# Optimization experiments

Measured on AMD Instinct MI355X. Metric: run time of the kernel, lower is better.

## Reference

```python
import jax, jax.numpy as jnp
import numpy as np

ALPHA = 0.5
INV_COEFF = 25.0
STD_COEFF = 25.0
COV_COEFF = 1.0
NUM_MATCHES = 50
EPS = 1e-5
GAMMA = 1.0


def _cdist(a, b):
    # (B,M,C),(B,N,C) -> (B,M,N) euclidean, matmul-based like torch.cdist
    a2 = jnp.sum(a * a, axis=-1, keepdims=True)            # (B,M,1)
    b2 = jnp.sum(b * b, axis=-1, keepdims=True)            # (B,N,1)
    d2 = a2 + jnp.swapaxes(b2, -1, -2) - 2.0 * jnp.einsum('bmc,bnc->bmn', a, b)
    return jnp.sqrt(jnp.maximum(d2, 0.0))


def _nn_match(input_maps, candidate_maps, distances, num_matches):
    # topk(k=1, largest=False) == min/argmin over last dim
    nn_dists = jnp.min(distances, axis=-1)                 # (B,M)
    nn_indices = jnp.argmin(distances, axis=-1)            # (B,M)
    # k smallest nn_dists, ascending order
    _, best_input_idx = jax.lax.top_k(-nn_dists, num_matches)   # (B,k)
    best_cand_idx = jnp.take_along_axis(nn_indices, best_input_idx, axis=1)
    filt_in = jnp.take_along_axis(input_maps, best_input_idx[:, :, None], axis=1)
    filt_cand = jnp.take_along_axis(candidate_maps, best_cand_idx[:, :, None], axis=1)
    return filt_in, filt_cand


def _off_diag_sq_sum(c):
    return jnp.sum(c * c) - jnp.sum(jnp.diag(c) ** 2)


def _std_term(x_flat):
    # unbiased variance over sample dim (torch var default)
    std = jnp.sqrt(jnp.var(x_flat, axis=0, ddof=1) + EPS)
    return jnp.mean(jax.nn.relu(GAMMA - std)) / 2.0


def _cov_term(x_flat):
    n, c = x_flat.shape
    xc = x_flat - jnp.mean(x_flat, axis=0)
    cov = xc.T @ xc / (n - 1)
    return _off_diag_sq_sum(cov) / c


def _vicreg_global(x, y):
    inv = jnp.mean((x - y) ** 2)
    std = _std_term(x) + _std_term(y)
    cov = _cov_term(x) + _cov_term(y)
    return INV_COEFF * inv + STD_COEFF * std + COV_COEFF * cov


def _vicregl_maps(x, y):
    # x, y: (B, k, C)
    inv = jnp.mean((x - y) ** 2)
    xf = x.reshape(-1, x.shape[-1])
    yf = y.reshape(-1, y.shape[-1])
    std = _std_term(xf) + _std_term(yf)
    cov = _cov_term(xf) + _cov_term(yf)
    return INV_COEFF * inv, STD_COEFF * std, COV_COEFF * cov


def _local_loss(spatial_1, spatial_2):
    B, C, H, W = spatial_1.shape
    maps_1 = spatial_1.reshape(B, C, H * W).transpose(0, 2, 1)   # (B,HW,C)
    maps_2 = spatial_2.reshape(B, C, H * W).transpose(0, 2, 1)
    d12 = _cdist(maps_1, maps_2)
    m1f, m1n = _nn_match(maps_1, maps_2, d12, NUM_MATCHES)
    d21 = _cdist(maps_2, maps_1)
    m2f, m2n = _nn_match(maps_2, maps_1, d21, NUM_MATCHES)
    inv1, var1, cov1 = _vicregl_maps(m1f, m1n)
    inv2, var2, cov2 = _vicregl_maps(m2f, m2n)
    return (inv1 + inv2) / 2 + (var1 + var2) / 2 + (cov1 + cov2) / 2


def setup_inputs() -> dict:
    key = jax.random.key(0)
    k1, k2, k3, k4 = jax.random.split(key, 4)
    B, C, H, W = 64, 768, 24, 24
    return {
        'spatial_1': jax.random.normal(k1, (B, C, H, W), dtype=jnp.float32),
        'pooled_1': jax.random.normal(k2, (B, C), dtype=jnp.float32),
        'spatial_2': jax.random.normal(k3, (B, C, H, W), dtype=jnp.float32),
        'pooled_2': jax.random.normal(k4, (B, C), dtype=jnp.float32),
    }


def reference(spatial_1, pooled_1, spatial_2, pooled_2):
    global_loss = _vicreg_global(pooled_1, pooled_2)
    local_loss = _local_loss(spatial_1, spatial_2)
    return ALPHA * global_loss + (1.0 - ALPHA) * local_loss
```

## Files before the change

kernel.cpp:

```cpp
#include <hip/hip_runtime.h>
#include <stdint.h>

typedef unsigned long long ull;
typedef unsigned int uint;
typedef unsigned short ushort;

typedef __attribute__((ext_vector_type(8))) short short8;
typedef __attribute__((ext_vector_type(4))) float floatx4;

#define B   64
#define C   768
#define HW  576
#define K   50
#define NLOC (B*K)

#define OFF_SLOTS   0
#define OFF_COLSUM  256
#define OFF_NN1     18688
#define OFF_NN2     313600
#define OFF_SELP    608512
#define OFF_SELQ    634112
#define OFF_XT      954624
#define OFF_MP      OFF_XT
#define OFF_XGT     114200832
#define OFF_M       133861632

#define SLOT_INVG 0
#define SLOT_STD  1
#define SLOT_COV  7
#define SLOT_INV1 13
#define SLOT_INV2 14

__device__ __forceinline__ ull umin64(ull a, ull b) { return a < b ? a : b; }

__device__ __forceinline__ float bf2f_lo(uint u) { return __uint_as_float(u << 16); }
__device__ __forceinline__ float bf2f_hi(uint u) { return __uint_as_float(u & 0xffff0000u); }
__device__ __forceinline__ float bf2f(ushort u) { return __uint_as_float(((uint)u) << 16); }

__device__ __forceinline__ ushort f2bf(float f) {
    uint u = __float_as_uint(f);
    uint r = (u + 0x7fffu + ((u >> 16) & 1u)) >> 16;
    return (ushort)r;
}

__device__ __forceinline__ float blk_reduce_sum(float v, float* s4) {
    for (int off = 32; off > 0; off >>= 1) v += __shfl_down(v, off, 64);
    int lane = threadIdx.x & 63, w = threadIdx.x >> 6;
    if (lane == 0) s4[w] = v;
    __syncthreads();
    float r = 0.f;
    if (threadIdx.x == 0) r = s4[0] + s4[1] + s4[2] + s4[3];
    return r;
}

__global__ __launch_bounds__(256) void convert_kernel(const float* __restrict__ x1,
                                                      const float* __restrict__ x2,
                                                      ushort* __restrict__ xT,
                                                      float* __restrict__ normp) {
    int z = blockIdx.y;
    int which = z >> 6, b = z & 63;
    int half = blockIdx.x & 1;
    int pt = blockIdx.x >> 1;
    int p0 = pt * 64, c0 = half * 384;
    const float* X = (which ? x2 : x1) + ((size_t)b * C + c0) * HW + p0;

    __shared__ ushort tile[64][392];
    __shared__ float nlds[64][4];

    int t = threadIdx.x;
    int pq = t & 15, cq = t >> 4;
    int w = t >> 6;

    float ss[4] = {0.f, 0.f, 0.f, 0.f};

#pragma unroll
    for (int pass = 0; pass < 6; ++pass) {
        floatx4 v[4];
#pragma unroll
        for (int i = 0; i < 4; ++i)
            v[i] = *(const floatx4*)(X + (size_t)(pass * 64 + 4 * cq + i) * HW + 4 * pq);
#pragma unroll
        for (int j = 0; j < 4; ++j) {
            ushort u0 = f2bf(v[0][j]), u1 = f2bf(v[1][j]);
            ushort u2 = f2bf(v[2][j]), u3 = f2bf(v[3][j]);
            ushort4 uu; uu.x = u0; uu.y = u1; uu.z = u2; uu.w = u3;
            *(ushort4*)&tile[4 * pq + j][pass * 64 + 4 * cq] = uu;
            float r0 = bf2f(u0), r1 = bf2f(u1), r2 = bf2f(u2), r3 = bf2f(u3);
            ss[j] = fmaf(r0, r0, ss[j]); ss[j] = fmaf(r1, r1, ss[j]);
            ss[j] = fmaf(r2, r2, ss[j]); ss[j] = fmaf(r3, r3, ss[j]);
        }
    }
#pragma unroll
    for (int j = 0; j < 4; ++j) {
        ss[j] += __shfl_xor(ss[j], 16, 64);
        ss[j] += __shfl_xor(ss[j], 32, 64);
    }
    if ((t & 63) < 16) {
#pragma unroll
        for (int j = 0; j < 4; ++j) nlds[4 * pq + j][w] = ss[j];
    }
    __syncthreads();

    ushort* dst = xT + (((size_t)which * B + b) * HW + p0) * C + c0;
    const char* tb = (const char*)tile;
#pragma unroll
    for (int step = 0; step < 12; ++step) {
        int ib = (step * 256 + t) * 16;
        int p = ib / 768, cb = ib % 768;
        short8 vv = *(const short8*)(tb + (size_t)p * 784 + cb);
        *(short8*)(dst + (size_t)p * C + (cb >> 1)) = vv;
    }
    if (t < 64) {
        float nv = nlds[t][0] + nlds[t][1] + nlds[t][2] + nlds[t][3];
        normp[((size_t)half * 128 + which * 64 + b) * HW + p0 + t] = nv;
    }
}

template<int NG>
__device__ __forceinline__ void gemm_pp(const ushort* const (&gA)[2], const ushort* const (&gB)[2],
                                        char* pool, int w,
                                        const int (&offA)[4], const int (&offB)[4],
                                        floatx4 (&acc)[4][4]) {
    auto issue = [&](int h) {
        char* buf = pool + (h & 3) * 16384;
#pragma unroll
        for (int n = 0; n < 2; ++n) {
            __builtin_amdgcn_global_load_lds(
                (const __attribute__((address_space(1))) void*)(gA[n] + h * 32),
                (__attribute__((address_space(3))) void*)(buf + w * 2048 + n * 1024), 16, 0, 0);
            __builtin_amdgcn_global_load_lds(
                (const __attribute__((address_space(1))) void*)(gB[n] + h * 32),
                (__attribute__((address_space(3))) void*)(buf + 8192 + w * 2048 + n * 1024), 16, 0, 0);
        }
    };
    issue(0); issue(1); issue(2);
    for (int h = 0; h < NG; ++h) {
        if (h < NG - 2)      asm volatile("s_waitcnt vmcnt(8)" ::: "memory");
        else if (h == NG - 2) asm volatile("s_waitcnt vmcnt(4)" ::: "memory");
        else                  asm volatile("s_waitcnt vmcnt(0)" ::: "memory");
        __builtin_amdgcn_s_barrier();
        if (h + 3 < NG) issue(h + 3);
        __builtin_amdgcn_sched_barrier(0);
        const char* buf = pool + (h & 3) * 16384;
        short8 a[4], bb[4];
#pragma unroll
        for (int i = 0; i < 4; ++i) a[i] = *(const short8*)(buf + offA[i]);
#pragma unroll
        for (int j = 0; j < 4; ++j) bb[j] = *(const short8*)(buf + 8192 + offB[j]);
#pragma unroll
        for (int i = 0; i < 4; ++i)
#pragma unroll
            for (int j = 0; j < 4; ++j)
                acc[i][j] = __builtin_amdgcn_mfma_f32_16x16x32_bf16(a[i], bb[j], acc[i][j], 0, 0, 0);
    }
}

__global__ __launch_bounds__(256) void cdist_mfma(const ushort* __restrict__ xT,
                                                  const float* __restrict__ normp,
                                                  ull* __restrict__ nn1,
                                                  ull* __restrict__ nn2) {
    int id = blockIdx.x;
    int xcd = id & 7, slot = id >> 3;
    int b = xcd + 8 * (slot / 25);
    int t = slot % 25;
    int qt = t % 5, pt = t / 5;

    const ushort* X1 = xT + (size_t)b * HW * C;
    const ushort* X2 = xT + (size_t)(B + b) * HW * C;

    __shared__ ull pool[8192];
    char* poolc = (char*)pool;

    int tid = threadIdx.x;
    int w = tid >> 6, l = tid & 63;
    int quad = l >> 4, col = l & 15;
    int lrow = l >> 2, pos = l & 3;

    const ushort* gA[2]; const ushort* gB[2];
#pragma unroll
    for (int n = 0; n < 2; ++n) {
        int sm = w * 32 + n * 16 + lrow;
        int cdat = pos ^ ((sm >> 1) & 3);
        int p = pt * 128 + sm; if (p >= HW) p = HW - 1;
        int q = qt * 128 + sm; if (q >= HW) q = HW - 1;
        gA[n] = X1 + (size_t)p * C + cdat * 8;
        gB[n] = X2 + (size_t)q * C + cdat * 8;
    }

    int offA[4], offB[4];
#pragma unroll
    for (int i = 0; i < 4; ++i) {
        int m_loc = (w >> 1) * 64 + i * 16 + col;
        offA[i] = m_loc * 64 + ((quad ^ ((m_loc >> 1) & 3)) * 16);
        int n_loc = (w & 1) * 64 + i * 16 + col;
        offB[i] = n_loc * 64 + ((quad ^ ((n_loc >> 1) & 3)) * 16);
    }

    floatx4 zero = {0.f, 0.f, 0.f, 0.f};
    floatx4 acc[4][4];
#pragma unroll
    for (int i = 0; i < 4; ++i)
#pragma unroll
        for (int j = 0; j < 4; ++j) acc[i][j] = zero;

    gemm_pp<24>(gA, gB, poolc, w, offA, offB, acc);

    const float* n1a = normp + (size_t)b * HW;
    const float* n1b = normp + (size_t)(128 + b) * HW;
    const float* n2a = normp + (size_t)(64 + b) * HW;
    const float* n2b = normp + (size_t)(192 + b) * HW;
    float n1v[4][4]; bool vp[4][4];
    float n2v[4];    bool vq[4];
#pragma unroll
    for (int i = 0; i < 4; ++i)
#pragma unroll
        for (int r = 0; r < 4; ++r) {
            int p = pt * 128 + (w >> 1) * 64 + i * 16 + quad * 4 + r;
            vp[i][r] = (p < HW);
            int pc = p < HW ? p : (HW - 1);
            n1v[i][r] = n1a[pc] + n1b[pc];
        }
#pragma unroll
    for (int j = 0; j < 4; ++j) {
        int q = qt * 128 + (w & 1) * 64 + j * 16 + col;
        vq[j] = (q < HW);
        int qc = q < HW ? q : (HW - 1);
        n2v[j] = n2a[qc] + n2b[qc];
    }

    __syncthreads();
    typedef ull row33[33];
    row33* red = (row33*)pool;

#pragma unroll
    for (int i = 0; i < 4; ++i)
#pragma unroll
        for (int r = 0; r < 4; ++r) {
            int p_loc = (w >> 1) * 64 + i * 16 + quad * 4 + r;
            ull best = ~0ull;
#pragma unroll
            for (int j = 0; j < 4; ++j) {
                if (!vq[j]) continue;
                float d2 = fmaxf(n1v[i][r] + n2v[j] - 2.0f * acc[i][j][r], 0.0f);
                unsigned q_glob = qt * 128 + (w & 1) * 64 + j * 16 + col;
                best = umin64(best, ((ull)__float_as_uint(d2) << 32) | q_glob);
            }
            red[p_loc][(w & 1) * 16 + col] = best;
        }
    __syncthreads();
    if (tid < 128) {
        int p_glob = pt * 128 + tid;
        ull m = ~0ull;
#pragma unroll
        for (int x = 0; x < 32; ++x) m = umin64(m, red[tid][x]);
        if (p_glob < HW) atomicMin(&nn1[(size_t)b * HW + p_glob], m);
    }
    __syncthreads();
#pragma unroll
    for (int j = 0; j < 4; ++j) {
        int q_loc = (w & 1) * 64 + j * 16 + col;
        ull best = ~0ull;
#pragma unroll
        for (int i = 0; i < 4; ++i)
#pragma unroll
            for (int r = 0; r < 4; ++r) {
                if (!vp[i][r]) continue;
                float d2 = fmaxf(n1v[i][r] + n2v[j] - 2.0f * acc[i][j][r], 0.0f);
                unsigned p_glob = pt * 128 + (w >> 1) * 64 + i * 16 + quad * 4 + r;
                best = umin64(best, ((ull)__float_as_uint(d2) << 32) | p_glob);
            }
        red[q_loc][(w >> 1) * 4 + quad] = best;
    }
    __syncthreads();
    if (tid < 128) {
        int q_glob = qt * 128 + tid;
        ull m = ~0ull;
#pragma unroll
        for (int x = 0; x < 8; ++x) m = umin64(m, red[tid][x]);
        if (q_glob < HW) atomicMin(&nn2[(size_t)b * HW + q_glob], m);
    }
}

__global__ __launch_bounds__(64) void select_topk_wave(const ull* __restrict__ nn1,
                                                       const ull* __restrict__ nn2,
                                                       int* __restrict__ sel_p,
                                                       int* __restrict__ sel_q) {
    int b = blockIdx.x, dir = blockIdx.y;
    const ull* nn = dir ? nn2 : nn1;
    int lane = threadIdx.x;
    ull key[9]; uint qv[9];
#pragma unroll
    for (int r = 0; r < 9; ++r) {
        int p = r * 64 + lane;
        ull e = nn[(size_t)b * HW + p];
        key[r] = (e & 0xFFFFFFFF00000000ull) | (unsigned)p;
        qv[r] = (uint)(e & 0xFFFFFFFFu);
    }
    int* sp = sel_p + (dir * B + b) * K;
    int* sq = sel_q + (dir * B + b) * K;
    for (int it = 0; it < K; ++it) {
        ull m = key[0];
#pragma unroll
        for (int r = 1; r < 9; ++r) m = umin64(m, key[r]);
#pragma unroll
        for (int off = 32; off > 0; off >>= 1) m = umin64(m, __shfl_xor(m, off, 64));
#pragma unroll
        for (int r = 0; r < 9; ++r) {
            if (key[r] == m) {
                sp[it] = (int)(uint)(m & 0xFFFFFFFFu);
                sq[it] = (int)qv[r];
                key[r] = ~0ull;
            }
        }
    }
}

__global__ __launch_bounds__(256) void gather_jmajor(const ushort* __restrict__ xT,
                                                     const int* __restrict__ sel_p,
                                                     const int* __restrict__ sel_q,
                                                     ushort* __restrict__ XgT) {
    int j = blockIdx.x, s = blockIdx.y;
    int dir = s >> 1;
    int whichsrc = (s == 1 || s == 2) ? 1 : 0;
    const int* sel = (s & 1) ? sel_q : sel_p;
    __shared__ int sidx[64];
    __shared__ uint buf[64][33];
    int tid = threadIdx.x;
    if (tid < 64) sidx[tid] = sel[(dir * B + tid) * K + j];
    __syncthreads();
    int rb = tid >> 2, u = tid & 3;
    const ushort* srow = xT + (((size_t)whichsrc * B + rb) * HW + sidx[rb]) * C;
    int wv = tid >> 6, lb = tid & 63;
    ushort* obase = XgT + (size_t)s * C * NLOC + (size_t)j * 64 + lb;
    for (int ch = 0; ch < 12; ++ch) {
        __syncthreads();
        uint4 v0 = *(const uint4*)(srow + ch * 64 + u * 8);
        uint4 v1 = *(const uint4*)(srow + ch * 64 + (u + 4) * 8);
        buf[rb][u * 4 + 0] = v0.x; buf[rb][u * 4 + 1] = v0.y;
        buf[rb][u * 4 + 2] = v0.z; buf[rb][u * 4 + 3] = v0.w;
        buf[rb][(u + 4) * 4 + 0] = v1.x; buf[rb][(u + 4) * 4 + 1] = v1.y;
        buf[rb][(u + 4) * 4 + 2] = v1.z; buf[rb][(u + 4) * 4 + 3] = v1.w;
        __syncthreads();
#pragma unroll
        for (int st = 0; st < 16; ++st) {
            int cl = wv + st * 4;
            uint uv = buf[lb][cl >> 1];
            ushort val = (cl & 1) ? (ushort)(uv >> 16) : (ushort)(uv & 0xffffu);
            obase[(size_t)(ch * 64 + cl) * NLOC] = val;
        }
    }
}

__global__ __launch_bounds__(256) void ata_mfma(const ushort* __restrict__ XgT,
                                                float* __restrict__ Mp) {
    int bx = blockIdx.x;
    int mat = blockIdx.y, split = blockIdx.z;
    int rt = bx / 6, ct = bx % 6;
    const ushort* X = XgT + (size_t)mat * C * NLOC;

    __shared__ ull pool[8192];
    char* poolc = (char*)pool;

    int tid = threadIdx.x;
    int w = tid >> 6, l = tid & 63;
    int quad = l >> 4, col = l & 15;
    int lrow = l >> 2, pos = l & 3;

    const ushort* gA[2]; const ushort* gB[2];
#pragma unroll
    for (int n = 0; n < 2; ++n) {
        int sm = w * 32 + n * 16 + lrow;
        int cdat = pos ^ ((sm >> 1) & 3);
        gA[n] = X + (size_t)(rt * 128 + sm) * NLOC + split * 640 + cdat * 8;
        gB[n] = X + (size_t)(ct * 128 + sm) * NLOC + split * 640 + cdat * 8;
    }

    int offA[4], offB[4];
#pragma unroll
    for (int i = 0; i < 4; ++i) {
        int m_loc = (w >> 1) * 64 + i * 16 + col;
        offA[i] = m_loc * 64 + ((quad ^ ((m_loc >> 1) & 3)) * 16);
        int n_loc = (w & 1) * 64 + i * 16 + col;
        offB[i] = n_loc * 64 + ((quad ^ ((n_loc >> 1) & 3)) * 16);
    }

    floatx4 zero = {0.f, 0.f, 0.f, 0.f};
    floatx4 acc[4][4];
#pragma unroll
    for (int i = 0; i < 4; ++i)
#pragma unroll
        for (int j = 0; j < 4; ++j) acc[i][j] = zero;

    gemm_pp<20>(gA, gB, poolc, w, offA, offB, acc);

    float* Mo = Mp + (size_t)(mat * 5 + split) * C * C;
#pragma unroll
    for (int i = 0; i < 4; ++i)
#pragma unroll
        for (int j = 0; j < 4; ++j)
#pragma unroll
            for (int r = 0; r < 4; ++r) {
                int row = rt * 128 + (w >> 1) * 64 + i * 16 + quad * 4 + r;
                int cc  = ct * 128 + (w & 1) * 64 + j * 16 + col;
                Mo[(size_t)row * C + cc] = acc[i][j][r];
            }
}

__global__ __launch_bounds__(256) void ata_pooled(const float* __restrict__ p1,
                                                  const float* __restrict__ p2,
                                                  float* __restrict__ M) {
    int mat = 4 + blockIdx.z;
    const float* X = (mat == 4) ? p1 : p2;
    int n = B;
    float* Mo = M + (size_t)mat * C * C;
    int ct = blockIdx.x, rt = blockIdx.y;

    __shared__ float As[16][64];
    __shared__ float Bs[16][64];
    int tid = threadIdx.x;
    int tx = tid & 15, ty = tid >> 4;
    int lr = tid >> 4, lc = (tid & 15) * 4;

    float acc[4][4] = {};
    for (int k0 = 0; k0 < n; k0 += 16) {
        float4 av = *(const float4*)&X[(size_t)(k0 + lr) * C + rt * 64 + lc];
        float4 bv = *(const float4*)&X[(size_t)(k0 + lr) * C + ct * 64 + lc];
        __syncthreads();
        *(float4*)&As[lr][lc] = av;
        *(float4*)&Bs[lr][lc] = bv;
        __syncthreads();
#pragma unroll
        for (int kk = 0; kk < 16; ++kk) {
            float4 af = *(const float4*)&As[kk][ty * 4];
            float4 bf = *(const float4*)&Bs[kk][tx * 4];
            float a[4] = {af.x, af.y, af.z, af.w};
            float bb[4] = {bf.x, bf.y, bf.z, bf.w};
#pragma unroll
            for (int i = 0; i < 4; ++i)
#pragma unroll
                for (int j = 0; j < 4; ++j)
                    acc[i][j] = fmaf(a[i], bb[j], acc[i][j]);
        }
    }
#pragma unroll
    for (int i = 0; i < 4; ++i) {
        float4 o = {acc[i][0], acc[i][1], acc[i][2], acc[i][3]};
        *(float4*)&Mo[(size_t)(rt * 64 + ty * 4 + i) * C + ct * 64 + tx * 4] = o;
    }
}

__global__ __launch_bounds__(256) void colsum4_kernel(const ushort* __restrict__ XgT,
                                                      float* __restrict__ colsum) {
    int mat = blockIdx.y, cb = blockIdx.x * 4;
    int r = threadIdx.x >> 6, lane = threadIdx.x & 63;
    const ushort* row = XgT + ((size_t)mat * C + cb + r) * NLOC;
    float s = 0.f;
    for (int i = lane; i < NLOC; i += 64) s += bf2f(row[i]);
    for (int off = 32; off > 0; off >>= 1) s += __shfl_down(s, off, 64);
    if (lane == 0) colsum[mat * C + cb + r] = s;
}

__global__ __launch_bounds__(256) void colsum_pooled(const float* __restrict__ p1,
                                                     const float* __restrict__ p2,
                                                     float* __restrict__ colsum) {
    int mat = 4 + blockIdx.y;
    const float* X = (mat == 4) ? p1 : p2;
    int c = blockIdx.x * 256 + threadIdx.x;
    float s = 0.f;
    for (int r = 0; r < B; ++r) s += X[(size_t)r * C + c];
    colsum[mat * C + c] = s;
}

__global__ __launch_bounds__(256) void std_kernel(const float* __restrict__ Mp,
                                                  const float* __restrict__ M,
                                                  const float* __restrict__ colsum,
                                                  float* __restrict__ slots) {
    int mat = blockIdx.y;
    float n = (mat < 4) ? (float)NLOC : (float)B;
    int c = blockIdx.x * 256 + threadIdx.x;
    float r = 0.f;
    if (c < C) {
        float mcc;
        if (mat < 4) {
            mcc = 0.f;
#pragma unroll
            for (int s = 0; s < 5; ++s)
                mcc += Mp[(size_t)(mat * 5 + s) * C * C + (size_t)c * C + c];
        } else {
            mcc = M[(size_t)mat * C * C + (size_t)c * C + c];
        }
        float cs = colsum[mat * C + c];
        float var = (mcc - cs * cs / n) / (n - 1.0f);
        float sd = sqrtf(var + 1e-5f);
        float g = 1.0f - sd;
        r = g > 0.f ? g : 0.f;
    }
    __shared__ float s4[4];
    float t = blk_reduce_sum(r, s4);
    if (threadIdx.x == 0) atomicAdd(&slots[SLOT_STD + mat], t);
}

__global__ __launch_bounds__(256) void cov_kernel(const float* __restrict__ Mp,
                                                  const float* __restrict__ M,
                                                  const float* __restrict__ colsum,
                                                  float* __restrict__ slots) {
    int mat = blockIdx.y;
    float n = (mat < 4) ? (float)NLOC : (float)B;
    float invn1 = 1.0f / (n - 1.0f);
    __shared__ float cs_s[C];
    for (int c = threadIdx.x; c < C; c += 256) cs_s[c] = colsum[mat * C + c];
    __syncthreads();
    float s = 0.f;
    int r0 = blockIdx.x * 16;
    for (int r = 0; r < 16; ++r) {
        int row = r0 + r;
        float csr = cs_s[row] / n;
        if (mat < 4) {
            const float* Mr0 = Mp + (size_t)(mat * 5 + 0) * C * C + (size_t)row * C;
            const float* Mr1 = Mp + (size_t)(mat * 5 + 1) * C * C + (size_t)row * C;
            const float* Mr2 = Mp + (size_t)(mat * 5 + 2) * C * C + (size_t)row * C;
            const float* Mr3 = Mp + (size_t)(mat * 5 + 3) * C * C + (size_t)row * C;
            const float* Mr4 = Mp + (size_t)(mat * 5 + 4) * C * C + (size_t)row * C;
            for (int c = threadIdx.x; c < C; c += 256) {
                float v = Mr0[c];
                v += Mr1[c]; v += Mr2[c]; v += Mr3[c]; v += Mr4[c];
                float cv = (v - csr * cs_s[c]) * invn1;
                if (c != row) s = fmaf(cv, cv, s);
            }
        } else {
            const float* Mr = M + (size_t)mat * C * C + (size_t)row * C;
            for (int c = threadIdx.x; c < C; c += 256) {
                float cv = (Mr[c] - csr * cs_s[c]) * invn1;
                if (c != row) s = fmaf(cv, cv, s);
            }
        }
    }
    __shared__ float s4[4];
    float t = blk_reduce_sum(s, s4);
    if (threadIdx.x == 0) atomicAdd(&slots[SLOT_COV + mat], t);
}

__global__ __launch_bounds__(256) void inv_global_kernel(const float* __restrict__ p1,
                                                         const float* __restrict__ p2,
                                                         float* __restrict__ slots) {
    int idx = blockIdx.x * 256 + threadIdx.x;
    int stride = gridDim.x * 256;
    float s = 0.f;
    for (int i = idx; i < B * C; i += stride) {
        float d = p1[i] - p2[i];
        s = fmaf(d, d, s);
    }
    __shared__ float s4[4];
    float t = blk_reduce_sum(s, s4);
    if (threadIdx.x == 0) atomicAdd(&slots[SLOT_INVG], t);
}

__global__ __launch_bounds__(256) void inv_local2(const ushort* __restrict__ XgT,
                                                  float* __restrict__ slots) {
    int pair = blockIdx.y;
    const uint* A4 = (const uint*)(XgT + (size_t)(2 * pair) * C * NLOC);
    const uint* B4 = (const uint*)(XgT + (size_t)(2 * pair + 1) * C * NLOC);
    int idx = blockIdx.x * 256 + threadIdx.x;
    int stride = gridDim.x * 256;
    int n = C * NLOC / 2;
    float s = 0.f;
    for (int i = idx; i < n; i += stride) {
        uint ua = A4[i], ub = B4[i];
        float d0 = bf2f_lo(ua) - bf2f_lo(ub);
        float d1 = bf2f_hi(ua) - bf2f_hi(ub);
        s = fmaf(d0, d0, s);
        s = fmaf(d1, d1, s);
    }
    __shared__ float s4[4];
    float t = blk_reduce_sum(s, s4);
    if (threadIdx.x == 0) atomicAdd(&slots[(pair == 0) ? SLOT_INV1 : SLOT_INV2], t);
}

__global__ void final_kernel(const float* __restrict__ slots, float* __restrict__ out) {
    float std_t[6], cov_t[6];
    for (int m = 0; m < 6; ++m) {
        std_t[m] = slots[SLOT_STD + m] / (float)C * 0.5f;
        cov_t[m] = slots[SLOT_COV + m] / (float)C;
    }
    float inv_g = slots[SLOT_INVG] / (float)(B * C);
    float global_loss = 25.0f * inv_g + 25.0f * (std_t[4] + std_t[5]) + (cov_t[4] + cov_t[5]);
    float inv1 = 25.0f * slots[SLOT_INV1] / (float)(NLOC * C);
    float inv2 = 25.0f * slots[SLOT_INV2] / (float)(NLOC * C);
    float var1 = 25.0f * (std_t[0] + std_t[1]);
    float var2 = 25.0f * (std_t[2] + std_t[3]);
    float cov1 = cov_t[0] + cov_t[1];
    float cov2 = cov_t[2] + cov_t[3];
    float local_loss = (inv1 + inv2) * 0.5f + (var1 + var2) * 0.5f + (cov1 + cov2) * 0.5f;
    out[0] = 0.5f * global_loss + 0.5f * local_loss;
}

extern "C" void kernel_launch(void* const* d_in, const int* in_sizes, int n_in,
                              void* d_out, int out_size, void* d_ws, size_t ws_size,
                              hipStream_t stream) {
    const float* spatial_1 = (const float*)d_in[0];
    const float* pooled_1  = (const float*)d_in[1];
    const float* spatial_2 = (const float*)d_in[2];
    const float* pooled_2  = (const float*)d_in[3];
    float* out = (float*)d_out;

    char* ws = (char*)d_ws;
    float*  slots  = (float*)(ws + OFF_SLOTS);
    float*  colsum = (float*)(ws + OFF_COLSUM);
    ull*    nn1    = (ull*)(ws + OFF_NN1);
    ull*    nn2    = (ull*)(ws + OFF_NN2);
    int*    sel_p  = (int*)(ws + OFF_SELP);
    int*    sel_q  = (int*)(ws + OFF_SELQ);
    ushort* xT     = (ushort*)(ws + OFF_XT);
    float*  Mp     = (float*)(ws + OFF_MP);
    ushort* XgT    = (ushort*)(ws + OFF_XGT);
    float*  M      = (float*)(ws + OFF_M);
    float*  normp  = (float*)(ws + OFF_M);

    hipMemsetAsync(ws, 0, OFF_NN1, stream);
    hipMemsetAsync(ws + OFF_NN1, 0xFF, OFF_SELP - OFF_NN1, stream);

    convert_kernel<<<dim3(18, 128), 256, 0, stream>>>(spatial_1, spatial_2, xT, normp);
    cdist_mfma<<<1600, 256, 0, stream>>>(xT, normp, nn1, nn2);
    select_topk_wave<<<dim3(B, 2), 64, 0, stream>>>(nn1, nn2, sel_p, sel_q);
    gather_jmajor<<<dim3(K, 4), 256, 0, stream>>>(xT, sel_p, sel_q, XgT);
    ata_mfma<<<dim3(36, 4, 5), 256, 0, stream>>>(XgT, Mp);
    ata_pooled<<<dim3(12, 12, 2), 256, 0, stream>>>(pooled_1, pooled_2, M);
    colsum4_kernel<<<dim3(192, 4), 256, 0, stream>>>(XgT, colsum);
    colsum_pooled<<<dim3(3, 2), 256, 0, stream>>>(pooled_1, pooled_2, colsum);
    std_kernel<<<dim3(3, 6), 256, 0, stream>>>(Mp, M, colsum, slots);
    cov_kernel<<<dim3(48, 6), 256, 0, stream>>>(Mp, M, colsum, slots);
    inv_global_kernel<<<dim3(96), 256, 0, stream>>>(pooled_1, pooled_2, slots);
    inv_local2<<<dim3(300, 2), 256, 0, stream>>>(XgT, slots);
    final_kernel<<<1, 1, 0, stream>>>(slots, out);
}
```

Measured before the change: 470.2 us.

## Shrink GEMM tiles to 64x128, raise occupancy, fuse colsum/std/inv reductions

The cdist and AᵀA MFMA kernels move from 128x128 to 64x128 tiles with a smaller LDS pool and launch bounds of 3 blocks per CU. The grid nearly doubles, which should improve occupancy and CU fill. The nn2 reduction now uses wave shuffles instead of an extra LDS pass. Several small kernels are fused: colsum and inv_local are merged into one scan, colsum_pooled goes into ata_pooled, and the std term goes into cov_kernel. This cuts launches and extra passes over XgT, at the cost of more tile-level reloads of A/B data from global memory.

```diff
diff --git a/kernel.cpp b/kernel.cpp
--- a/kernel.cpp
+++ b/kernel.cpp
@@ -117,58 +117,58 @@
 }
 
 template<int NG>
-__device__ __forceinline__ void gemm_pp(const ushort* const (&gA)[2], const ushort* const (&gB)[2],
-                                        char* pool, int w,
-                                        const int (&offA)[4], const int (&offB)[4],
-                                        floatx4 (&acc)[4][4]) {
+__device__ __forceinline__ void gemm_pp64(const ushort* gA, const ushort* gB0, const ushort* gB1,
+                                          char* pool, int w,
+                                          const int (&offA)[4], const int (&offB)[2],
+                                          floatx4 (&acc)[4][2]) {
     auto issue = [&](int h) {
-        char* buf = pool + (h & 3) * 16384;
-#pragma unroll
-        for (int n = 0; n < 2; ++n) {
-            __builtin_amdgcn_global_load_lds(
-                (const __attribute__((address_space(1))) void*)(gA[n] + h * 32),
-                (__attribute__((address_space(3))) void*)(buf + w * 2048 + n * 1024), 16, 0, 0);
-            __builtin_amdgcn_global_load_lds(
-                (const __attribute__((address_space(1))) void*)(gB[n] + h * 32),
-                (__attribute__((address_space(3))) void*)(buf + 8192 + w * 2048 + n * 1024), 16, 0, 0);
-        }
+        char* buf = pool + (h & 3) * 12288;
+        __builtin_amdgcn_global_load_lds(
+            (const __attribute__((address_space(1))) void*)(gA + h * 32),
+            (__attribute__((address_space(3))) void*)(buf + w * 1024), 16, 0, 0);
+        __builtin_amdgcn_global_load_lds(
+            (const __attribute__((address_space(1))) void*)(gB0 + h * 32),
+            (__attribute__((address_space(3))) void*)(buf + 4096 + w * 1024), 16, 0, 0);
+        __builtin_amdgcn_global_load_lds(
+            (const __attribute__((address_space(1))) void*)(gB1 + h * 32),
+            (__attribute__((address_space(3))) void*)(buf + 4096 + (4 + w) * 1024), 16, 0, 0);
     };
     issue(0); issue(1); issue(2);
     for (int h = 0; h < NG; ++h) {
-        if (h < NG - 2)      asm volatile("s_waitcnt vmcnt(8)" ::: "memory");
-        else if (h == NG - 2) asm volatile("s_waitcnt vmcnt(4)" ::: "memory");
+        if (h < NG - 2)       asm volatile("s_waitcnt vmcnt(6)" ::: "memory");
+        else if (h == NG - 2) asm volatile("s_waitcnt vmcnt(3)" ::: "memory");
         else                  asm volatile("s_waitcnt vmcnt(0)" ::: "memory");
         __builtin_amdgcn_s_barrier();
         if (h + 3 < NG) issue(h + 3);
         __builtin_amdgcn_sched_barrier(0);
-        const char* buf = pool + (h & 3) * 16384;
-        short8 a[4], bb[4];
+        const char* buf = pool + (h & 3) * 12288;
+        short8 a[4], bb[2];
 #pragma unroll
         for (int i = 0; i < 4; ++i) a[i] = *(const short8*)(buf + offA[i]);
 #pragma unroll
-        for (int j = 0; j < 4; ++j) bb[j] = *(const short8*)(buf + 8192 + offB[j]);
+        for (int j = 0; j < 2; ++j) bb[j] = *(const short8*)(buf + offB[j]);
 #pragma unroll
         for (int i = 0; i < 4; ++i)
 #pragma unroll
-            for (int j = 0; j < 4; ++j)
+            for (int j = 0; j < 2; ++j)
                 acc[i][j] = __builtin_amdgcn_mfma_f32_16x16x32_bf16(a[i], bb[j], acc[i][j], 0, 0, 0);
     }
 }
 
-__global__ __launch_bounds__(256) void cdist_mfma(const ushort* __restrict__ xT,
-                                                  const float* __restrict__ normp,
-                                                  ull* __restrict__ nn1,
-                                                  ull* __restrict__ nn2) {
+__global__ __launch_bounds__(256, 3) void cdist_mfma(const ushort* __restrict__ xT,
+                                                     const float* __restrict__ normp,
+                                                     ull* __restrict__ nn1,
+                                                     ull* __restrict__ nn2) {
     int id = blockIdx.x;
     int xcd = id & 7, slot = id >> 3;
-    int b = xcd + 8 * (slot / 25);
-    int t = slot % 25;
+    int b = xcd + 8 * (slot / 45);
+    int t = slot % 45;
     int qt = t % 5, pt = t / 5;
 
     const ushort* X1 = xT + (size_t)b * HW * C;
     const ushort* X2 = xT + (size_t)(B + b) * HW * C;
 
-    __shared__ ull pool[8192];
+    __shared__ ull pool[6144];
     char* poolc = (char*)pool;
 
     int tid = threadIdx.x;
@@ -176,108 +176,101 @@
     int quad = l >> 4, col = l & 15;
     int lrow = l >> 2, pos = l & 3;
 
-    const ushort* gA[2]; const ushort* gB[2];
-#pragma unroll
-    for (int n = 0; n < 2; ++n) {
-        int sm = w * 32 + n * 16 + lrow;
-        int cdat = pos ^ ((sm >> 1) & 3);
-        int p = pt * 128 + sm; if (p >= HW) p = HW - 1;
-        int q = qt * 128 + sm; if (q >= HW) q = HW - 1;
-        gA[n] = X1 + (size_t)p * C + cdat * 8;
-        gB[n] = X2 + (size_t)q * C + cdat * 8;
-    }
-
-    int offA[4], offB[4];
+    int smA = w * 16 + lrow;
+    int cdatA = pos ^ ((smA >> 1) & 3);
+    const ushort* gA = X1 + (size_t)(pt * 64 + smA) * C + cdatA * 8;
+    int smB0 = w * 16 + lrow;
+    int cdatB0 = pos ^ ((smB0 >> 1) & 3);
+    int q0 = qt * 128 + smB0; if (q0 >= HW) q0 = HW - 1;
+    const ushort* gB0 = X2 + (size_t)q0 * C + cdatB0 * 8;
+    int smB1 = 64 + w * 16 + lrow;
+    int cdatB1 = pos ^ ((smB1 >> 1) & 3);
+    int q1 = qt * 128 + smB1; if (q1 >= HW) q1 = HW - 1;
+    const ushort* gB1 = X2 + (size_t)q1 * C + cdatB1 * 8;
+
+    int offA[4], offB[2];
 #pragma unroll
     for (int i = 0; i < 4; ++i) {
-        int m_loc = (w >> 1) * 64 + i * 16 + col;
-        offA[i] = m_loc * 64 + ((quad ^ ((m_loc >> 1) & 3)) * 16);
-        int n_loc = (w & 1) * 64 + i * 16 + col;
-        offB[i] = n_loc * 64 + ((quad ^ ((n_loc >> 1) & 3)) * 16);
+        int p_loc = i * 16 + col;
+        offA[i] = p_loc * 64 + ((quad ^ ((p_loc >> 1) & 3)) * 16);
+    }
+#pragma unroll
+    for (int j = 0; j < 2; ++j) {
+        int q_loc = w * 32 + j * 16 + col;
+        offB[j] = 4096 + q_loc * 64 + ((quad ^ ((q_loc >> 1) & 3)) * 16);
     }
 
     floatx4 zero = {0.f, 0.f, 0.f, 0.f};
-    floatx4 acc[4][4];
+    floatx4 acc[4][2];
 #pragma unroll
     for (int i = 0; i < 4; ++i)
 #pragma unroll
-        for (int j = 0; j < 4; ++j) acc[i][j] = zero;
-
-    gemm_pp<24>(gA, gB, poolc, w, offA, offB, acc);
+        for (int j = 0; j < 2; ++j) acc[i][j] = zero;
+
+    gemm_pp64<24>(gA, gB0, gB1, poolc, w, offA, offB, acc);
 
     const float* n1a = normp + (size_t)b * HW;
     const float* n1b = normp + (size_t)(128 + b) * HW;
     const float* n2a = normp + (size_t)(64 + b) * HW;
     const float* n2b = normp + (size_t)(192 + b) * HW;
-    float n1v[4][4]; bool vp[4][4];
-    float n2v[4];    bool vq[4];
+    float n1v[4][4];
+    float n2v[2]; bool vq[2]; int qg[2];
 #pragma unroll
     for (int i = 0; i < 4; ++i)
 #pragma unroll
         for (int r = 0; r < 4; ++r) {
-            int p = pt * 128 + (w >> 1) * 64 + i * 16 + quad * 4 + r;
-            vp[i][r] = (p < HW);
-            int pc = p < HW ? p : (HW - 1);
-            n1v[i][r] = n1a[pc] + n1b[pc];
+            int p = pt * 64 + i * 16 + quad * 4 + r;
+            n1v[i][r] = n1a[p] + n1b[p];
         }
 #pragma unroll
-    for (int j = 0; j < 4; ++j) {
-        int q = qt * 128 + (w & 1) * 64 + j * 16 + col;
+    for (int j = 0; j < 2; ++j) {
+        int q = qt * 128 + w * 32 + j * 16 + col;
+        qg[j] = q;
         vq[j] = (q < HW);
         int qc = q < HW ? q : (HW - 1);
         n2v[j] = n2a[qc] + n2b[qc];
     }
 
     __syncthreads();
-    typedef ull row33[33];
-    row33* red = (row33*)pool;
+    typedef ull row65[65];
+    row65* red = (row65*)pool;
 
 #pragma unroll
     for (int i = 0; i < 4; ++i)
 #pragma unroll
         for (int r = 0; r < 4; ++r) {
-            int p_loc = (w >> 1) * 64 + i * 16 + quad * 4 + r;
+            int p_loc = i * 16 + quad * 4 + r;
             ull best = ~0ull;
 #pragma unroll
-            for (int j = 0; j < 4; ++j) {
+            for (int j = 0; j < 2; ++j) {
                 if (!vq[j]) continue;
                 float d2 = fmaxf(n1v[i][r] + n2v[j] - 2.0f * acc[i][j][r], 0.0f);
-                unsigned q_glob = qt * 128 + (w & 1) * 64 + j * 16 + col;
-                best = umin64(best, ((ull)__float_as_uint(d2) << 32) | q_glob);
+                best = umin64(best, ((ull)__float_as_uint(d2) << 32) | (unsigned)qg[j]);
             }
-            red[p_loc][(w & 1) * 16 + col] = best;
+            red[p_loc][w * 16 + col] = best;
         }
     __syncthreads();
-    if (tid < 128) {
-        int p_glob = pt * 128 + tid;
+    if (tid < 64) {
         ull m = ~0ull;
 #pragma unroll
-        for (int x = 0; x < 32; ++x) m = umin64(m, red[tid][x]);
-        if (p_glob < HW) atomicMin(&nn1[(size_t)b * HW + p_glob], m);
-    }
-    __syncthreads();
-#pragma unroll
-    for (int j = 0; j < 4; ++j) {
-        int q_loc = (w & 1) * 64 + j * 16 + col;
+        for (int x = 0; x < 64; ++x) m = umin64(m, red[tid][x]);
+        atomicMin(&nn1[(size_t)b * HW + pt * 64 + tid], m);
+    }
+#pragma unroll
+    for (int j = 0; j < 2; ++j) {
         ull best = ~0ull;
 #pragma unroll
         for (int i = 0; i < 4; ++i)
 #pragma unroll
             for (int r = 0; r < 4; ++r) {
-                if (!vp[i][r]) continue;
                 float d2 = fmaxf(n1v[i][r] + n2v[j] - 2.0f * acc[i][j][r], 0.0f);
-                unsigned p_glob = pt * 128 + (w >> 1) * 64 + i * 16 + quad * 4 + r;
+                unsigned p_glob = pt * 64 + i * 16 + quad * 4 + r;
                 best = umin64(best, ((ull)__float_as_uint(d2) << 32) | p_glob);
             }
-        red[q_loc][(w >> 1) * 4 + quad] = best;
-    }
-    __syncthreads();
-    if (tid < 128) {
-        int q_glob = qt * 128 + tid;
-        ull m = ~0ull;
-#pragma unroll
-        for (int x = 0; x < 8; ++x) m = umin64(m, red[tid][x]);
-        if (q_glob < HW) atomicMin(&nn2[(size_t)b * HW + q_glob], m);
+        best = umin64(best, __shfl_xor(best, 16, 64));
+        best = umin64(best, __shfl_xor(best, 32, 64));
+        if (quad == 0 && vq[j])
+            atomicMin(&nn2[(size_t)b * HW + qg[j]], best);
     }
 }
 
@@ -351,14 +344,14 @@
     }
 }
 
-__global__ __launch_bounds__(256) void ata_mfma(const ushort* __restrict__ XgT,
-                                                float* __restrict__ Mp) {
+__global__ __launch_bounds__(256, 3) void ata_mfma(const ushort* __restrict__ XgT,
+                                                   float* __restrict__ Mp) {
     int bx = blockIdx.x;
     int mat = blockIdx.y, split = blockIdx.z;
     int rt = bx / 6, ct = bx % 6;
     const ushort* X = XgT + (size_t)mat * C * NLOC;
 
-    __shared__ ull pool[8192];
+    __shared__ ull pool[6144];
     char* poolc = (char*)pool;
 
     int tid = threadIdx.x;
@@ -366,49 +359,54 @@
     int quad = l >> 4, col = l & 15;
     int lrow = l >> 2, pos = l & 3;
 
-    const ushort* gA[2]; const ushort* gB[2];
-#pragma unroll
-    for (int n = 0; n < 2; ++n) {
-        int sm = w * 32 + n * 16 + lrow;
-        int cdat = pos ^ ((sm >> 1) & 3);
-        gA[n] = X + (size_t)(rt * 128 + sm) * NLOC + split * 640 + cdat * 8;
-        gB[n] = X + (size_t)(ct * 128 + sm) * NLOC + split * 640 + cdat * 8;
-    }
-
-    int offA[4], offB[4];
+    int smA = w * 16 + lrow;
+    int cdatA = pos ^ ((smA >> 1) & 3);
+    const ushort* gA = X + (size_t)(rt * 64 + smA) * NLOC + split * 640 + cdatA * 8;
+    int smB0 = w * 16 + lrow;
+    int cdatB0 = pos ^ ((smB0 >> 1) & 3);
+    const ushort* gB0 = X + (size_t)(ct * 128 + smB0) * NLOC + split * 640 + cdatB0 * 8;
+    int smB1 = 64 + w * 16 + lrow;
+    int cdatB1 = pos ^ ((smB1 >> 1) & 3);
+    const ushort* gB1 = X + (size_t)(ct * 128 + smB1) * NLOC + split * 640 + cdatB1 * 8;
+
+    int offA[4], offB[2];
 #pragma unroll
     for (int i = 0; i < 4; ++i) {
-        int m_loc = (w >> 1) * 64 + i * 16 + col;
-        offA[i] = m_loc * 64 + ((quad ^ ((m_loc >> 1) & 3)) * 16);
-        int n_loc = (w & 1) * 64 + i * 16 + col;
-        offB[i] = n_loc * 64 + ((quad ^ ((n_loc >> 1) & 3)) * 16);
+        int p_loc = i * 16 + col;
+        offA[i] = p_loc * 64 + ((quad ^ ((p_loc >> 1) & 3)) * 16);
+    }
+#pragma unroll
+    for (int j = 0; j < 2; ++j) {
+        int q_loc = w * 32 + j * 16 + col;
+        offB[j] = 4096 + q_loc * 64 + ((quad ^ ((q_loc >> 1) & 3)) * 16);
     }
 
     floatx4 zero = {0.f, 0.f, 0.f, 0.f};
-    floatx4 acc[4][4];
+    floatx4 acc[4][2];
 #pragma unroll
     for (int i = 0; i < 4; ++i)
 #pragma unroll
-        for (int j = 0; j < 4; ++j) acc[i][j] = zero;
-
-    gemm_pp<20>(gA, gB, poolc, w, offA, offB, acc);
+        for (int j = 0; j < 2; ++j) acc[i][j] = zero;
+
+    gemm_pp64<20>(gA, gB0, gB1, poolc, w, offA, offB, acc);
 
     float* Mo = Mp + (size_t)(mat * 5 + split) * C * C;
 #pragma unroll
     for (int i = 0; i < 4; ++i)
 #pragma unroll
-        for (int j = 0; j < 4; ++j)
+        for (int j = 0; j < 2; ++j)
 #pragma unroll
             for (int r = 0; r < 4; ++r) {
-                int row = rt * 128 + (w >> 1) * 64 + i * 16 + quad * 4 + r;
-                int cc  = ct * 128 + (w & 1) * 64 + j * 16 + col;
+                int row = rt * 64 + i * 16 + quad * 4 + r;
+                int cc  = ct * 128 + w * 32 + j * 16 + col;
                 Mo[(size_t)row * C + cc] = acc[i][j][r];
             }
 }
 
 __global__ __launch_bounds__(256) void ata_pooled(const float* __restrict__ p1,
                                                   const float* __restrict__ p2,
-                                                  float* __restrict__ M) {
+                                                  float* __restrict__ M,
+                                                  float* __restrict__ colsum) {
     int mat = 4 + blockIdx.z;
     const float* X = (mat == 4) ? p1 : p2;
     int n = B;
@@ -447,57 +445,45 @@
         float4 o = {acc[i][0], acc[i][1], acc[i][2], acc[i][3]};
         *(float4*)&Mo[(size_t)(rt * 64 + ty * 4 + i) * C + ct * 64 + tx * 4] = o;
     }
-}
-
-__global__ __launch_bounds__(256) void colsum4_kernel(const ushort* __restrict__ XgT,
-                                                      float* __restrict__ colsum) {
-    int mat = blockIdx.y, cb = blockIdx.x * 4;
+    if (rt == 0 && tid < 64) {
+        int c = ct * 64 + tid;
+        float s = 0.f;
+        for (int r = 0; r < B; ++r) s += X[(size_t)r * C + c];
+        colsum[(size_t)mat * C + c] = s;
+    }
+}
+
+__global__ __launch_bounds__(256) void xgt_scan(const ushort* __restrict__ XgT,
+                                                float* __restrict__ colsum,
+                                                float* __restrict__ slots) {
+    int pair = blockIdx.y;
+    int cb = blockIdx.x * 4;
     int r = threadIdx.x >> 6, lane = threadIdx.x & 63;
-    const ushort* row = XgT + ((size_t)mat * C + cb + r) * NLOC;
-    float s = 0.f;
-    for (int i = lane; i < NLOC; i += 64) s += bf2f(row[i]);
-    for (int off = 32; off > 0; off >>= 1) s += __shfl_down(s, off, 64);
-    if (lane == 0) colsum[mat * C + cb + r] = s;
-}
-
-__global__ __launch_bounds__(256) void colsum_pooled(const float* __restrict__ p1,
-                                                     const float* __restrict__ p2,
-                                                     float* __restrict__ colsum) {
-    int mat = 4 + blockIdx.y;
-    const float* X = (mat == 4) ? p1 : p2;
-    int c = blockIdx.x * 256 + threadIdx.x;
-    float s = 0.f;
-    for (int r = 0; r < B; ++r) s += X[(size_t)r * C + c];
-    colsum[mat * C + c] = s;
-}
-
-__global__ __launch_bounds__(256) void std_kernel(const float* __restrict__ Mp,
-                                                  const float* __restrict__ M,
-                                                  const float* __restrict__ colsum,
-                                                  float* __restrict__ slots) {
-    int mat = blockIdx.y;
-    float n = (mat < 4) ? (float)NLOC : (float)B;
-    int c = blockIdx.x * 256 + threadIdx.x;
-    float r = 0.f;
-    if (c < C) {
-        float mcc;
-        if (mat < 4) {
-            mcc = 0.f;
-#pragma unroll
-            for (int s = 0; s < 5; ++s)
-                mcc += Mp[(size_t)(mat * 5 + s) * C * C + (size_t)c * C + c];
-        } else {
-            mcc = M[(size_t)mat * C * C + (size_t)c * C + c];
-        }
-        float cs = colsum[mat * C + c];
-        float var = (mcc - cs * cs / n) / (n - 1.0f);
-        float sd = sqrtf(var + 1e-5f);
-        float g = 1.0f - sd;
-        r = g > 0.f ? g : 0.f;
+    int c = cb + r;
+    const ushort* rowA = XgT + ((size_t)(2 * pair) * C + c) * NLOC;
+    const ushort* rowB = XgT + ((size_t)(2 * pair + 1) * C + c) * NLOC;
+    float sa = 0.f, sb = 0.f, sinv = 0.f;
+    for (int k = 0; k < K; ++k) {
+        int i = lane + 64 * k;
+        float a = bf2f(rowA[i]);
+        float b = bf2f(rowB[i]);
+        sa += a;
+        sb += b;
+        float d = a - b;
+        sinv = fmaf(d, d, sinv);
+    }
+    float ra = sa, rb = sb;
+    for (int off = 32; off > 0; off >>= 1) {
+        ra += __shfl_down(ra, off, 64);
+        rb += __shfl_down(rb, off, 64);
+    }
+    if (lane == 0) {
+        colsum[(2 * pair) * C + c] = ra;
+        colsum[(2 * pair + 1) * C + c] = rb;
     }
     __shared__ float s4[4];
-    float t = blk_reduce_sum(r, s4);
-    if (threadIdx.x == 0) atomicAdd(&slots[SLOT_STD + mat], t);
+    float t = blk_reduce_sum(sinv, s4);
+    if (threadIdx.x == 0) atomicAdd(&slots[(pair == 0) ? SLOT_INV1 : SLOT_INV2], t);
 }
 
 __global__ __launch_bounds__(256) void cov_kernel(const float* __restrict__ Mp,
@@ -510,7 +496,7 @@
     __shared__ float cs_s[C];
     for (int c = threadIdx.x; c < C; c += 256) cs_s[c] = colsum[mat * C + c];
     __syncthreads();
-    float s = 0.f;
+    float s = 0.f, s_std = 0.f;
     int r0 = blockIdx.x * 16;
     for (int r = 0; r < 16; ++r) {
         int row = r0 + r;
@@ -524,20 +510,40 @@
             for (int c = threadIdx.x; c < C; c += 256) {
                 float v = Mr0[c];
                 v += Mr1[c]; v += Mr2[c]; v += Mr3[c]; v += Mr4[c];
-                float cv = (v - csr * cs_s[c]) * invn1;
-                if (c != row) s = fmaf(cv, cv, s);
+                if (c != row) {
+                    float cv = (v - csr * cs_s[c]) * invn1;
+                    s = fmaf(cv, cv, s);
+                } else {
+                    float cs = cs_s[row];
+                    float var = (v - cs * cs / n) / (n - 1.0f);
+                    float sd = sqrtf(var + 1e-5f);
+                    float g = 1.0f - sd;
+                    s_std += (g > 0.f) ? g : 0.f;
+                }
             }
         } else {
             const float* Mr = M + (size_t)mat * C * C + (size_t)row * C;
             for (int c = threadIdx.x; c < C; c += 256) {
-                float cv = (Mr[c] - csr * cs_s[c]) * invn1;
-                if (c != row) s = fmaf(cv, cv, s);
+                float v = Mr[c];
+                if (c != row) {
+                    float cv = (v - csr * cs_s[c]) * invn1;
+                    s = fmaf(cv, cv, s);
+                } else {
+                    float cs = cs_s[row];
+                    float var = (v - cs * cs / n) / (n - 1.0f);
+                    float sd = sqrtf(var + 1e-5f);
+                    float g = 1.0f - sd;
+                    s_std += (g > 0.f) ? g : 0.f;
+                }
             }
         }
     }
     __shared__ float s4[4];
     float t = blk_reduce_sum(s, s4);
     if (threadIdx.x == 0) atomicAdd(&slots[SLOT_COV + mat], t);
+    __syncthreads();
+    float t2 = blk_reduce_sum(s_std, s4);
+    if (threadIdx.x == 0) atomicAdd(&slots[SLOT_STD + mat], t2);
 }
 
 __global__ __launch_bounds__(256) void inv_global_kernel(const float* __restrict__ p1,
@@ -553,27 +559,6 @@
     __shared__ float s4[4];
     float t = blk_reduce_sum(s, s4);
     if (threadIdx.x == 0) atomicAdd(&slots[SLOT_INVG], t);
-}
-
-__global__ __launch_bounds__(256) void inv_local2(const ushort* __restrict__ XgT,
-                                                  float* __restrict__ slots) {
-    int pair = blockIdx.y;
-    const uint* A4 = (const uint*)(XgT + (size_t)(2 * pair) * C * NLOC);
-    const uint* B4 = (const uint*)(XgT + (size_t)(2 * pair + 1) * C * NLOC);
-    int idx = blockIdx.x * 256 + threadIdx.x;
-    int stride = gridDim.x * 256;
-    int n = C * NLOC / 2;
-    float s = 0.f;
-    for (int i = idx; i < n; i += stride) {
-        uint ua = A4[i], ub = B4[i];
-        float d0 = bf2f_lo(ua) - bf2f_lo(ub);
-        float d1 = bf2f_hi(ua) - bf2f_hi(ub);
-        s = fmaf(d0, d0, s);
-        s = fmaf(d1, d1, s);
-    }
-    __shared__ float s4[4];
-    float t = blk_reduce_sum(s, s4);
-    if (threadIdx.x == 0) atomicAdd(&slots[(pair == 0) ? SLOT_INV1 : SLOT_INV2], t);
 }
 
 __global__ void final_kernel(const float* __restrict__ slots, float* __restrict__ out) {
@@ -620,16 +605,13 @@
     hipMemsetAsync(ws + OFF_NN1, 0xFF, OFF_SELP - OFF_NN1, stream);
 
     convert_kernel<<<dim3(18, 128), 256, 0, stream>>>(spatial_1, spatial_2, xT, normp);
-    cdist_mfma<<<1600, 256, 0, stream>>>(xT, normp, nn1, nn2);
+    cdist_mfma<<<2880, 256, 0, stream>>>(xT, normp, nn1, nn2);
     select_topk_wave<<<dim3(B, 2), 64, 0, stream>>>(nn1, nn2, sel_p, sel_q);
     gather_jmajor<<<dim3(K, 4), 256, 0, stream>>>(xT, sel_p, sel_q, XgT);
-    ata_mfma<<<dim3(36, 4, 5), 256, 0, stream>>>(XgT, Mp);
-    ata_pooled<<<dim3(12, 12, 2), 256, 0, stream>>>(pooled_1, pooled_2, M);
-    colsum4_kernel<<<dim3(192, 4), 256, 0, stream>>>(XgT, colsum);
-    colsum_pooled<<<dim3(3, 2), 256, 0, stream>>>(pooled_1, pooled_2, colsum);
-    std_kernel<<<dim3(3, 6), 256, 0, stream>>>(Mp, M, colsum, slots);
+    ata_mfma<<<dim3(72, 4, 5), 256, 0, stream>>>(XgT, Mp);
+    ata_pooled<<<dim3(12, 12, 2), 256, 0, stream>>>(pooled_1, pooled_2, M, colsum);
+    xgt_scan<<<dim3(192, 2), 256, 0, stream>>>(XgT, colsum, slots);
     cov_kernel<<<dim3(48, 6), 256, 0, stream>>>(Mp, M, colsum, slots);
     inv_global_kernel<<<dim3(96), 256, 0, stream>>>(pooled_1, pooled_2, slots);
-    inv_local2<<<dim3(300, 2), 256, 0, stream>>>(XgT, slots);
     final_kernel<<<1, 1, 0, stream>>>(slots, out);
 }
```

Result: faster. 448.1 us (-4.7%).
